# Kernel tuning notes

Hardware: AMD Instinct MI355X
Metric: run time of the kernel (lower is better)

## Reference

```python
import jax, jax.numpy as jnp
import numpy as np

N_NODES = 50000
N_EDGES = 800000
D = 96        # node_dim
DE = 96       # edge_dim
K_HOPS = 4
K = 2         # module's k; uses edge_attr[:, k-1]


def setup_inputs() -> dict:
    key = jax.random.key(0)
    ks = jax.random.split(key, 12)
    s = 1.0 / np.sqrt(D)
    se = 1.0 / np.sqrt(DE)
    s2 = 1.0 / np.sqrt(2 * D)
    return {
        "V": jax.random.normal(ks[0], (N_NODES, D), jnp.float32),
        "V_in": jax.random.normal(ks[1], (N_NODES, D), jnp.float32),
        "E": jax.random.normal(ks[2], (N_EDGES, DE), jnp.float32),
        "edge_attr": jax.random.uniform(ks[3], (N_EDGES, K_HOPS), jnp.float32),
        "src": jax.random.randint(ks[4], (N_EDGES,), 0, N_NODES),
        "dst": jax.random.randint(ks[5], (N_EDGES,), 0, N_NODES),
        # NodePooling linear A: node_dim -> node_dim
        "A_w": jax.random.uniform(ks[6], (D, D), jnp.float32, -s, s),
        "A_b": jax.random.uniform(ks[7], (D,), jnp.float32, -s, s),
        # M: edge_dim -> node_dim
        "M_w": jax.random.uniform(ks[8], (DE, D), jnp.float32, -se, se),
        "M_b": jax.random.uniform(ks[9], (D,), jnp.float32, -se, se),
        # W: 2*node_dim -> node_dim
        "W_w": jax.random.uniform(ks[10], (2 * D, D), jnp.float32, -s2, s2),
        "W_b": jax.random.uniform(ks[11], (D,), jnp.float32, -s2, s2),
    }


def reference(V, V_in, E, edge_attr, src, dst, A_w, A_b, M_w, M_b, W_w, W_b):
    # V = LeakyReLU(V, 0.2)
    V = jax.nn.leaky_relu(V, negative_slope=0.2)
    # NodePooling: ReLU(Linear(V))
    Vp = jax.nn.relu(V @ A_w + A_b)                      # [N, D]
    # edge projection
    Ep = E @ M_w + M_b                                   # [M, D]
    khop = edge_attr[:, K - 1:K]                         # [M, 1]
    # message: (src['V'] + data['E']) * KHOP, then sum-aggregate to dst
    msg = (Vp[src] + Ep) * khop                          # [M, D]
    agg = jax.ops.segment_sum(msg, dst, num_segments=N_NODES)  # [N, D]
    # cat aggregate with V_in, project, relu
    out = jax.nn.relu(jnp.concatenate([agg, V_in], axis=-1) @ W_w + W_b)
    return out
```

## Files before the change

kernel.cpp:

```cpp
#include <hip/hip_runtime.h>
#include <hip/hip_bf16.h>

#define NN 50000
#define NE 800000
#define DD 96
#define SVP 100
#define CAP 64

typedef float f4 __attribute__((ext_vector_type(4)));
typedef int   i4 __attribute__((ext_vector_type(4)));

__global__ __launch_bounds__(256) void k_vp(
    const float* __restrict__ V, const float* __restrict__ Aw,
    const float* __restrict__ Ab, float* __restrict__ Vp,
    int* __restrict__ cnt)
{
    __shared__ float sW[DD * DD];
    __shared__ float sV[64 * SVP];
    __shared__ float sB[DD];

    const int tid = threadIdx.x;
    const int gt = blockIdx.x * 256 + tid;
    if (gt < NN) cnt[gt] = 0;

    for (int i = tid; i < DD * DD / 4; i += 256)
        reinterpret_cast<f4*>(sW)[i] = reinterpret_cast<const f4*>(Aw)[i];
    if (tid < DD / 4)
        reinterpret_cast<f4*>(sB)[tid] = reinterpret_cast<const f4*>(Ab)[tid];

    const int row0 = blockIdx.x * 64;
    const int nr = min(64, NN - row0);
    for (int i = tid; i < nr * (DD / 4); i += 256) {
        const int r = i / (DD / 4);
        const int c = i % (DD / 4);
        f4 v = reinterpret_cast<const f4*>(V + (size_t)(row0 + r) * DD)[c];
        v[0] = v[0] > 0.f ? v[0] : 0.2f * v[0];
        v[1] = v[1] > 0.f ? v[1] : 0.2f * v[1];
        v[2] = v[2] > 0.f ? v[2] : 0.2f * v[2];
        v[3] = v[3] > 0.f ? v[3] : 0.2f * v[3];
        reinterpret_cast<f4*>(sV + r * SVP)[c] = v;
    }
    __syncthreads();

    const int cg = tid & 15;
    const int rg = tid >> 4;
    const int c0 = cg * 6;
    const int r0 = rg * 4;

    float acc[4][6];
#pragma unroll
    for (int rr = 0; rr < 4; ++rr)
#pragma unroll
        for (int j = 0; j < 6; ++j) acc[rr][j] = sB[c0 + j];

#pragma unroll 4
    for (int k = 0; k < DD; ++k) {
        float x[4];
#pragma unroll
        for (int rr = 0; rr < 4; ++rr) x[rr] = sV[(r0 + rr) * SVP + k];
#pragma unroll
        for (int j = 0; j < 6; ++j) {
            const float w = sW[k * DD + c0 + j];
#pragma unroll
            for (int rr = 0; rr < 4; ++rr)
                acc[rr][j] = fmaf(x[rr], w, acc[rr][j]);
        }
    }

#pragma unroll
    for (int rr = 0; rr < 4; ++rr) {
        const int row = row0 + r0 + rr;
        if (row < NN) {
#pragma unroll
            for (int j = 0; j < 6; ++j)
                Vp[(size_t)row * DD + c0 + j] = fmaxf(acc[rr][j], 0.f);
        }
    }
}

__global__ __launch_bounds__(256) void k_scatter(
    const int* __restrict__ src, const int* __restrict__ dst,
    const float* __restrict__ ea, int* __restrict__ cnt,
    i4* __restrict__ aux)
{
    const int e = blockIdx.x * 256 + threadIdx.x;
    if (e >= NE) return;
    const int d = dst[e];
    const int pos = atomicAdd(&cnt[d], 1);
    i4 a;
    a.x = src[e];
    a.y = e;
    a.z = __float_as_int(ea[(size_t)e * 4 + 1]);
    a.w = 0;
    if (pos < CAP)
        __builtin_nontemporal_store(a, aux + (size_t)d * CAP + pos);
}

__global__ __launch_bounds__(256, 4) void k_aggout(
    const float* __restrict__ Vp, const float* __restrict__ E,
    const int* __restrict__ cnt, const i4* __restrict__ aux,
    const float* __restrict__ Vin, const float* __restrict__ Mw,
    const float* __restrict__ Mb, const float* __restrict__ Ww,
    const float* __restrict__ Wb, float* __restrict__ out)
{
    __shared__ float sAgg[32 * SVP];
    __shared__ float sG[32 * SVP];
    __shared__ float sW[32 * DD];
    __shared__ float sB[DD];
    __shared__ float sS[32];

    const int tid = threadIdx.x;
    const int row0 = blockIdx.x * 32;

    {
        const int grp = tid >> 5;
        const int gl = tid & 31;
        const bool act = (gl < 24);

        i4 apre[4];
        int n[4];
#pragma unroll
        for (int i = 0; i < 4; ++i) {
            const int node = row0 + grp * 4 + i;
            const bool ok = (node < NN);
            apre[i] = ok ? __builtin_nontemporal_load(aux + (size_t)node * CAP + gl)
                         : i4{0, 0, 0, 0};
            n[i] = ok ? min(cnt[node], CAP) : 0;
        }

#pragma unroll
        for (int i = 0; i < 4; ++i) {
            const int nl = grp * 4 + i;
            const int node = row0 + nl;
            if (node >= NN) break;

            f4 av = {0.f, 0.f, 0.f, 0.f};
            f4 ag = {0.f, 0.f, 0.f, 0.f};
            float wsum = 0.f;

            i4 a = apre[i];
            const int nfirst = min(n[i], 32);

            int j = 0;
            for (; j + 8 <= nfirst; j += 8) {
                int ss[8], ee[8];
                float ww[8];
#pragma unroll
                for (int q = 0; q < 8; ++q) {
                    ss[q] = __shfl(a.x, j + q, 32);
                    ee[q] = __shfl(a.y, j + q, 32);
                    ww[q] = __shfl(__int_as_float(a.z), j + q, 32);
                }
                f4 Ev[8], Vv[8];
#pragma unroll
                for (int q = 0; q < 8; ++q) {
                    if (act) {
                        Ev[q] = __builtin_nontemporal_load(
                            reinterpret_cast<const f4*>(E + (size_t)ee[q] * DD) + gl);
                        Vv[q] = *(reinterpret_cast<const f4*>(Vp + (size_t)ss[q] * DD) + gl);
                    } else {
                        Ev[q] = f4{0, 0, 0, 0};
                        Vv[q] = f4{0, 0, 0, 0};
                    }
                }
#pragma unroll
                for (int q = 0; q < 8; ++q) {
#pragma unroll
                    for (int c = 0; c < 4; ++c) {
                        av[c] = fmaf(ww[q], Vv[q][c], av[c]);
                        ag[c] = fmaf(ww[q], Ev[q][c], ag[c]);
                    }
                    wsum += ww[q];
                }
            }
            for (; j + 4 <= nfirst; j += 4) {
                int ss[4], ee[4];
                float ww[4];
#pragma unroll
                for (int q = 0; q < 4; ++q) {
                    ss[q] = __shfl(a.x, j + q, 32);
                    ee[q] = __shfl(a.y, j + q, 32);
                    ww[q] = __shfl(__int_as_float(a.z), j + q, 32);
                }
                f4 Ev[4], Vv[4];
#pragma unroll
                for (int q = 0; q < 4; ++q) {
                    if (act) {
                        Ev[q] = __builtin_nontemporal_load(
                            reinterpret_cast<const f4*>(E + (size_t)ee[q] * DD) + gl);
                        Vv[q] = *(reinterpret_cast<const f4*>(Vp + (size_t)ss[q] * DD) + gl);
                    } else {
                        Ev[q] = f4{0, 0, 0, 0};
                        Vv[q] = f4{0, 0, 0, 0};
                    }
                }
#pragma unroll
                for (int q = 0; q < 4; ++q) {
#pragma unroll
                    for (int c = 0; c < 4; ++c) {
                        av[c] = fmaf(ww[q], Vv[q][c], av[c]);
                        ag[c] = fmaf(ww[q], Ev[q][c], ag[c]);
                    }
                    wsum += ww[q];
                }
            }
            for (; j < nfirst; ++j) {
                const int s0 = __shfl(a.x, j, 32), e0 = __shfl(a.y, j, 32);
                const float w0 = __shfl(__int_as_float(a.z), j, 32);
                f4 E0 = {0, 0, 0, 0}, V0 = {0, 0, 0, 0};
                if (act) {
                    E0 = __builtin_nontemporal_load(
                        reinterpret_cast<const f4*>(E + (size_t)e0 * DD) + gl);
                    V0 = *(reinterpret_cast<const f4*>(Vp + (size_t)s0 * DD) + gl);
                }
#pragma unroll
                for (int c = 0; c < 4; ++c) {
                    av[c] = fmaf(w0, V0[c], av[c]);
                    ag[c] = fmaf(w0, E0[c], ag[c]);
                }
                wsum += w0;
            }

            if (n[i] > 32) {
                i4 a2 = __builtin_nontemporal_load(
                    aux + (size_t)node * CAP + 32 + gl);
                const int rem = n[i] - 32;
                for (int jj = 0; jj < rem; ++jj) {
                    const int s0 = __shfl(a2.x, jj, 32), e0 = __shfl(a2.y, jj, 32);
                    const float w0 = __shfl(__int_as_float(a2.z), jj, 32);
                    f4 E0 = {0, 0, 0, 0}, V0 = {0, 0, 0, 0};
                    if (act) {
                        E0 = __builtin_nontemporal_load(
                            reinterpret_cast<const f4*>(E + (size_t)e0 * DD) + gl);
                        V0 = *(reinterpret_cast<const f4*>(Vp + (size_t)s0 * DD) + gl);
                    }
#pragma unroll
                    for (int c = 0; c < 4; ++c) {
                        av[c] = fmaf(w0, V0[c], av[c]);
                        ag[c] = fmaf(w0, E0[c], ag[c]);
                    }
                    wsum += w0;
                }
            }

            if (act) {
                *reinterpret_cast<f4*>(sAgg + nl * SVP + gl * 4) = av;
                *reinterpret_cast<f4*>(sG + nl * SVP + gl * 4) = ag;
            }
            if (gl == 0) sS[nl] = wsum;
        }
    }
    __syncthreads();

    const int cg = tid & 15;
    const int rg = tid >> 4;
    const int c0 = cg * 6;
    const int r0 = rg * 2;

    auto loadW = [&](const float* wsrc) {
        for (int i = tid; i < 32 * DD / 4; i += 256)
            reinterpret_cast<f4*>(sW)[i] = reinterpret_cast<const f4*>(wsrc)[i];
    };
    auto loadB = [&](const float* bsrc) {
        if (tid < DD / 4)
            reinterpret_cast<f4*>(sB)[tid] = reinterpret_cast<const f4*>(bsrc)[tid];
    };

    loadW(Mw); loadB(Mb);
    __syncthreads();

    float a[2][6];
#pragma unroll
    for (int rr = 0; rr < 2; ++rr) {
        const float sv = sS[r0 + rr];
#pragma unroll
        for (int j = 0; j < 6; ++j)
            a[rr][j] = sAgg[(r0 + rr) * SVP + c0 + j] + sv * sB[c0 + j];
    }
#pragma unroll
    for (int ch = 0; ch < 3; ++ch) {
        if (ch) {
            __syncthreads();
            loadW(Mw + ch * 32 * DD);
            __syncthreads();
        }
        const int kb = ch * 32;
#pragma unroll 4
        for (int k = 0; k < 32; ++k) {
            const float x0 = sG[r0 * SVP + kb + k];
            const float x1 = sG[(r0 + 1) * SVP + kb + k];
#pragma unroll
            for (int j = 0; j < 6; ++j) {
                const float w = sW[k * DD + c0 + j];
                a[0][j] = fmaf(x0, w, a[0][j]);
                a[1][j] = fmaf(x1, w, a[1][j]);
            }
        }
    }
    __syncthreads();
#pragma unroll
    for (int rr = 0; rr < 2; ++rr)
#pragma unroll
        for (int j = 0; j < 6; ++j)
            sAgg[(r0 + rr) * SVP + c0 + j] = a[rr][j];

    {
        const int nr = min(32, NN - row0);
        __syncthreads();
        for (int i = tid; i < nr * (DD / 4); i += 256) {
            const int r = i / (DD / 4);
            const int c = i % (DD / 4);
            reinterpret_cast<f4*>(sG + r * SVP)[c] =
                reinterpret_cast<const f4*>(Vin + (size_t)(row0 + r) * DD)[c];
        }
    }

    loadW(Ww); loadB(Wb);
    __syncthreads();

    float o[2][6];
#pragma unroll
    for (int rr = 0; rr < 2; ++rr)
#pragma unroll
        for (int j = 0; j < 6; ++j) o[rr][j] = sB[c0 + j];
#pragma unroll
    for (int ch = 0; ch < 3; ++ch) {
        if (ch) {
            __syncthreads();
            loadW(Ww + ch * 32 * DD);
            __syncthreads();
        }
        const int kb = ch * 32;
#pragma unroll 4
        for (int k = 0; k < 32; ++k) {
            const float x0 = sAgg[r0 * SVP + kb + k];
            const float x1 = sAgg[(r0 + 1) * SVP + kb + k];
#pragma unroll
            for (int j = 0; j < 6; ++j) {
                const float w = sW[k * DD + c0 + j];
                o[0][j] = fmaf(x0, w, o[0][j]);
                o[1][j] = fmaf(x1, w, o[1][j]);
            }
        }
    }

#pragma unroll
    for (int ch = 0; ch < 3; ++ch) {
        __syncthreads();
        loadW(Ww + (size_t)(96 + ch * 32) * DD);
        __syncthreads();
        const int kb = ch * 32;
#pragma unroll 4
        for (int k = 0; k < 32; ++k) {
            const float x0 = sG[r0 * SVP + kb + k];
            const float x1 = sG[(r0 + 1) * SVP + kb + k];
#pragma unroll
            for (int j = 0; j < 6; ++j) {
                const float w = sW[k * DD + c0 + j];
                o[0][j] = fmaf(x0, w, o[0][j]);
                o[1][j] = fmaf(x1, w, o[1][j]);
            }
        }
    }

#pragma unroll
    for (int rr = 0; rr < 2; ++rr) {
        const int row = row0 + r0 + rr;
        if (row < NN) {
#pragma unroll
            for (int j = 0; j < 6; ++j)
                out[(size_t)row * DD + c0 + j] = fmaxf(o[rr][j], 0.f);
        }
    }
}

extern "C" void kernel_launch(void* const* d_in, const int* in_sizes, int n_in,
                              void* d_out, int out_size, void* d_ws, size_t ws_size,
                              hipStream_t stream)
{
    const float* V   = (const float*)d_in[0];
    const float* Vin = (const float*)d_in[1];
    const float* E   = (const float*)d_in[2];
    const float* ea  = (const float*)d_in[3];
    const int*   src = (const int*)d_in[4];
    const int*   dst = (const int*)d_in[5];
    const float* Aw  = (const float*)d_in[6];
    const float* Ab  = (const float*)d_in[7];
    const float* Mw  = (const float*)d_in[8];
    const float* Mb  = (const float*)d_in[9];
    const float* Ww  = (const float*)d_in[10];
    const float* Wb  = (const float*)d_in[11];
    float* out = (float*)d_out;

    float* Vp  = (float*)d_ws;
    int*   cnt = (int*)(Vp + (size_t)NN * DD);
    size_t aux_off = (size_t)NN * DD + NN;
    aux_off = (aux_off + 3) & ~(size_t)3;
    i4*    aux = (i4*)((float*)d_ws + aux_off);

    k_vp<<<(NN + 63) / 64, 256, 0, stream>>>(V, Aw, Ab, Vp, cnt);
    k_scatter<<<(NE + 255) / 256, 256, 0, stream>>>(src, dst, ea, cnt, aux);
    k_aggout<<<(NN + 31) / 32, 256, 0, stream>>>(Vp, E, cnt, aux, Vin,
                                                 Mw, Mb, Ww, Wb, out);
}
```

Baseline: 226.9 us.

## Store Vp in fp16, shrink weight chunks, raise occupancy, use nontemporal I/O

Stores the intermediate node projection Vp as half precision, which halves the bytes moved by the random gather of source-node rows in the aggregation kernel. It also cuts the shared weight chunk from 32 to 12 rows so less LDS is used and launch bounds can ask for 5 blocks per CU. Vin loads and output stores become nontemporal and vectorised, and one barrier is dropped. In exchange, fp16 rounding adds precision error to Vp, and the smaller chunks mean more barrier-separated weight reloads.

After: 374.5 us. 65.0% more time.

```diff
diff --git a/kernel.cpp b/kernel.cpp
--- a/kernel.cpp
+++ b/kernel.cpp
@@ -1,18 +1,23 @@
 #include <hip/hip_runtime.h>
-#include <hip/hip_bf16.h>
+#include <hip/hip_fp16.h>
 
 #define NN 50000
 #define NE 800000
 #define DD 96
 #define SVP 100
 #define CAP 64
+#define KCH 12
+#define NCH 8
 
 typedef float f4 __attribute__((ext_vector_type(4)));
+typedef float f2 __attribute__((ext_vector_type(2)));
 typedef int   i4 __attribute__((ext_vector_type(4)));
+typedef _Float16 h4 __attribute__((ext_vector_type(4)));
+typedef _Float16 h2 __attribute__((ext_vector_type(2)));
 
 __global__ __launch_bounds__(256) void k_vp(
     const float* __restrict__ V, const float* __restrict__ Aw,
-    const float* __restrict__ Ab, float* __restrict__ Vp,
+    const float* __restrict__ Ab, _Float16* __restrict__ Vp,
     int* __restrict__ cnt)
 {
     __shared__ float sW[DD * DD];
@@ -71,9 +76,14 @@
     for (int rr = 0; rr < 4; ++rr) {
         const int row = row0 + r0 + rr;
         if (row < NN) {
-#pragma unroll
-            for (int j = 0; j < 6; ++j)
-                Vp[(size_t)row * DD + c0 + j] = fmaxf(acc[rr][j], 0.f);
+            h2* vph = reinterpret_cast<h2*>(Vp + (size_t)row * DD);
+#pragma unroll
+            for (int p = 0; p < 3; ++p) {
+                h2 hp;
+                hp[0] = (_Float16)fmaxf(acc[rr][2 * p], 0.f);
+                hp[1] = (_Float16)fmaxf(acc[rr][2 * p + 1], 0.f);
+                vph[c0 / 2 + p] = hp;
+            }
         }
     }
 }
@@ -96,8 +106,8 @@
         __builtin_nontemporal_store(a, aux + (size_t)d * CAP + pos);
 }
 
-__global__ __launch_bounds__(256, 4) void k_aggout(
-    const float* __restrict__ Vp, const float* __restrict__ E,
+__global__ __launch_bounds__(256, 5) void k_aggout(
+    const _Float16* __restrict__ Vp, const float* __restrict__ E,
     const int* __restrict__ cnt, const i4* __restrict__ aux,
     const float* __restrict__ Vin, const float* __restrict__ Mw,
     const float* __restrict__ Mb, const float* __restrict__ Ww,
@@ -105,7 +115,7 @@
 {
     __shared__ float sAgg[32 * SVP];
     __shared__ float sG[32 * SVP];
-    __shared__ float sW[32 * DD];
+    __shared__ float sW[KCH * DD];
     __shared__ float sB[DD];
     __shared__ float sS[32];
 
@@ -157,7 +167,10 @@
                     if (act) {
                         Ev[q] = __builtin_nontemporal_load(
                             reinterpret_cast<const f4*>(E + (size_t)ee[q] * DD) + gl);
-                        Vv[q] = *(reinterpret_cast<const f4*>(Vp + (size_t)ss[q] * DD) + gl);
+                        const h4 hv = *(reinterpret_cast<const h4*>(
+                            Vp + (size_t)ss[q] * DD) + gl);
+                        Vv[q] = f4{(float)hv[0], (float)hv[1],
+                                   (float)hv[2], (float)hv[3]};
                     } else {
                         Ev[q] = f4{0, 0, 0, 0};
                         Vv[q] = f4{0, 0, 0, 0};
@@ -188,7 +201,10 @@
                     if (act) {
                         Ev[q] = __builtin_nontemporal_load(
                             reinterpret_cast<const f4*>(E + (size_t)ee[q] * DD) + gl);
-                        Vv[q] = *(reinterpret_cast<const f4*>(Vp + (size_t)ss[q] * DD) + gl);
+                        const h4 hv = *(reinterpret_cast<const h4*>(
+                            Vp + (size_t)ss[q] * DD) + gl);
+                        Vv[q] = f4{(float)hv[0], (float)hv[1],
+                                   (float)hv[2], (float)hv[3]};
                     } else {
                         Ev[q] = f4{0, 0, 0, 0};
                         Vv[q] = f4{0, 0, 0, 0};
@@ -211,7 +227,9 @@
                 if (act) {
                     E0 = __builtin_nontemporal_load(
                         reinterpret_cast<const f4*>(E + (size_t)e0 * DD) + gl);
-                    V0 = *(reinterpret_cast<const f4*>(Vp + (size_t)s0 * DD) + gl);
+                    const h4 hv = *(reinterpret_cast<const h4*>(
+                        Vp + (size_t)s0 * DD) + gl);
+                    V0 = f4{(float)hv[0], (float)hv[1], (float)hv[2], (float)hv[3]};
                 }
 #pragma unroll
                 for (int c = 0; c < 4; ++c) {
@@ -232,7 +250,9 @@
                     if (act) {
                         E0 = __builtin_nontemporal_load(
                             reinterpret_cast<const f4*>(E + (size_t)e0 * DD) + gl);
-                        V0 = *(reinterpret_cast<const f4*>(Vp + (size_t)s0 * DD) + gl);
+                        const h4 hv = *(reinterpret_cast<const h4*>(
+                            Vp + (size_t)s0 * DD) + gl);
+                        V0 = f4{(float)hv[0], (float)hv[1], (float)hv[2], (float)hv[3]};
                     }
 #pragma unroll
                     for (int c = 0; c < 4; ++c) {
@@ -258,7 +278,7 @@
     const int r0 = rg * 2;
 
     auto loadW = [&](const float* wsrc) {
-        for (int i = tid; i < 32 * DD / 4; i += 256)
+        for (int i = tid; i < KCH * DD / 4; i += 256)
             reinterpret_cast<f4*>(sW)[i] = reinterpret_cast<const f4*>(wsrc)[i];
     };
     auto loadB = [&](const float* bsrc) {
@@ -278,15 +298,15 @@
             a[rr][j] = sAgg[(r0 + rr) * SVP + c0 + j] + sv * sB[c0 + j];
     }
 #pragma unroll
-    for (int ch = 0; ch < 3; ++ch) {
+    for (int ch = 0; ch < NCH; ++ch) {
         if (ch) {
             __syncthreads();
-            loadW(Mw + ch * 32 * DD);
+            loadW(Mw + ch * KCH * DD);
             __syncthreads();
         }
-        const int kb = ch * 32;
-#pragma unroll 4
-        for (int k = 0; k < 32; ++k) {
+        const int kb = ch * KCH;
+#pragma unroll
+        for (int k = 0; k < KCH; ++k) {
             const float x0 = sG[r0 * SVP + kb + k];
             const float x1 = sG[(r0 + 1) * SVP + kb + k];
 #pragma unroll
@@ -306,12 +326,11 @@
 
     {
         const int nr = min(32, NN - row0);
-        __syncthreads();
         for (int i = tid; i < nr * (DD / 4); i += 256) {
             const int r = i / (DD / 4);
             const int c = i % (DD / 4);
-            reinterpret_cast<f4*>(sG + r * SVP)[c] =
-                reinterpret_cast<const f4*>(Vin + (size_t)(row0 + r) * DD)[c];
+            reinterpret_cast<f4*>(sG + r * SVP)[c] = __builtin_nontemporal_load(
+                reinterpret_cast<const f4*>(Vin + (size_t)(row0 + r) * DD) + c);
         }
     }
 
@@ -324,15 +343,15 @@
 #pragma unroll
         for (int j = 0; j < 6; ++j) o[rr][j] = sB[c0 + j];
 #pragma unroll
-    for (int ch = 0; ch < 3; ++ch) {
+    for (int ch = 0; ch < NCH; ++ch) {
         if (ch) {
             __syncthreads();
-            loadW(Ww + ch * 32 * DD);
+            loadW(Ww + ch * KCH * DD);
             __syncthreads();
         }
-        const int kb = ch * 32;
-#pragma unroll 4
-        for (int k = 0; k < 32; ++k) {
+        const int kb = ch * KCH;
+#pragma unroll
+        for (int k = 0; k < KCH; ++k) {
             const float x0 = sAgg[r0 * SVP + kb + k];
             const float x1 = sAgg[(r0 + 1) * SVP + kb + k];
 #pragma unroll
@@ -345,13 +364,13 @@
     }
 
 #pragma unroll
-    for (int ch = 0; ch < 3; ++ch) {
+    for (int ch = 0; ch < NCH; ++ch) {
         __syncthreads();
-        loadW(Ww + (size_t)(96 + ch * 32) * DD);
+        loadW(Ww + (size_t)(DD + ch * KCH) * DD);
         __syncthreads();
-        const int kb = ch * 32;
-#pragma unroll 4
-        for (int k = 0; k < 32; ++k) {
+        const int kb = ch * KCH;
+#pragma unroll
+        for (int k = 0; k < KCH; ++k) {
             const float x0 = sG[r0 * SVP + kb + k];
             const float x1 = sG[(r0 + 1) * SVP + kb + k];
 #pragma unroll
@@ -367,9 +386,14 @@
     for (int rr = 0; rr < 2; ++rr) {
         const int row = row0 + r0 + rr;
         if (row < NN) {
-#pragma unroll
-            for (int j = 0; j < 6; ++j)
-                out[(size_t)row * DD + c0 + j] = fmaxf(o[rr][j], 0.f);
+            float* op = out + (size_t)row * DD + c0;
+#pragma unroll
+            for (int p = 0; p < 3; ++p) {
+                f2 v;
+                v[0] = fmaxf(o[rr][2 * p], 0.f);
+                v[1] = fmaxf(o[rr][2 * p + 1], 0.f);
+                __builtin_nontemporal_store(v, reinterpret_cast<f2*>(op) + p);
+            }
         }
     }
 }
@@ -392,11 +416,11 @@
     const float* Wb  = (const float*)d_in[11];
     float* out = (float*)d_out;
 
-    float* Vp  = (float*)d_ws;
-    int*   cnt = (int*)(Vp + (size_t)NN * DD);
-    size_t aux_off = (size_t)NN * DD + NN;
-    aux_off = (aux_off + 3) & ~(size_t)3;
-    i4*    aux = (i4*)((float*)d_ws + aux_off);
+    _Float16* Vp = (_Float16*)d_ws;
+    int* cnt = (int*)((char*)d_ws + (size_t)NN * DD * 2);
+    size_t aux_byte = (size_t)NN * DD * 2 + (size_t)NN * 4;
+    aux_byte = (aux_byte + 15) & ~(size_t)15;
+    i4* aux = (i4*)((char*)d_ws + aux_byte);
 
     k_vp<<<(NN + 63) / 64, 256, 0, stream>>>(V, Aw, Ab, Vp, cnt);
     k_scatter<<<(NE + 255) / 256, 256, 0, stream>>>(src, dst, ea, cnt, aux);
```
